# Kernel tuning notes

Hardware: AMD Instinct MI355X
Metric: run time of the kernel (lower is better)

The kernel has to match this reference:

```python
import jax, jax.numpy as jnp
import numpy as np
import math

D_MODEL, D_STATE, D_CONV = 1024, 16, 4
D_INNER = 2 * D_MODEL
DT_RANK = math.ceil(D_MODEL / 16)
B, L = 4, 2048


def setup_inputs() -> dict:
    key = jax.random.key(0)
    ks = jax.random.split(key, 10)
    s = 0.02
    x = jax.random.normal(ks[0], (B, L, D_MODEL), dtype=jnp.float32)
    ln_g = jnp.ones((D_MODEL,), jnp.float32)
    ln_b = jnp.zeros((D_MODEL,), jnp.float32)
    W_in = jax.random.normal(ks[1], (D_MODEL, 2 * D_INNER), jnp.float32) * s
    conv_w = jax.random.normal(ks[2], (D_INNER, 1, D_CONV), jnp.float32) * s
    conv_b = jnp.zeros((D_INNER,), jnp.float32)
    W_xp = jax.random.normal(ks[3], (D_INNER, DT_RANK + 2 * D_STATE), jnp.float32) * s
    W_dt = jax.random.normal(ks[4], (DT_RANK, D_INNER), jnp.float32) * (DT_RANK ** -0.5)
    # inverse-softplus of dt ~ 0.01 (between dt_min=0.001 and dt_max=0.1)
    dt_bias = jnp.full((D_INNER,), float(np.log(np.expm1(0.01))), jnp.float32)
    # S4D-real init: A = 1..d_state per channel
    A_log = jnp.log(jnp.broadcast_to(jnp.arange(1, D_STATE + 1, dtype=jnp.float32), (D_INNER, D_STATE)))
    D_skip = jnp.ones((D_INNER,), jnp.float32)
    W_out = jax.random.normal(ks[5], (D_INNER, D_MODEL), jnp.float32) * s
    return dict(x=x, ln_g=ln_g, ln_b=ln_b, W_in=W_in, conv_w=conv_w, conv_b=conv_b,
                W_xp=W_xp, W_dt=W_dt, dt_bias=dt_bias, A_log=A_log, D_skip=D_skip, W_out=W_out)


def _layernorm(x, g, b, eps=1e-5):
    m = jnp.mean(x, axis=-1, keepdims=True)
    v = jnp.mean(jnp.square(x - m), axis=-1, keepdims=True)
    return (x - m) * jax.lax.rsqrt(v + eps) * g + b


def _mamba(xn, W_in, conv_w, conv_b, W_xp, W_dt, dt_bias, A_log, D_skip, W_out):
    # xn: [B, L, d_model]
    xz = xn @ W_in                                   # [B, L, 2*d_inner]
    xi, z = jnp.split(xz, 2, axis=-1)                # each [B, L, d_inner]
    # depthwise causal conv over sequence
    xi_t = jnp.transpose(xi, (0, 2, 1))              # [B, d_inner, L]
    xc = jax.lax.conv_general_dilated(
        xi_t, conv_w, window_strides=(1,), padding=[(D_CONV - 1, 0)],
        feature_group_count=D_INNER, dimension_numbers=('NCH', 'OIH', 'NCH'))
    xc = jnp.transpose(xc, (0, 2, 1)) + conv_b       # [B, L, d_inner]
    xc = jax.nn.silu(xc)
    # input-dependent dt, B, C
    x_dbl = xc @ W_xp                                # [B, L, dt_rank + 2*d_state]
    dt_lo, Bm, Cm = jnp.split(x_dbl, [DT_RANK, DT_RANK + D_STATE], axis=-1)
    delta = jax.nn.softplus(dt_lo @ W_dt + dt_bias)  # [B, L, d_inner]
    A = -jnp.exp(A_log)                              # [d_inner, d_state]

    def step(h, inp):
        dt_t, B_t, C_t, u_t = inp                    # [B,D], [B,N], [B,N], [B,D]
        dA = jnp.exp(dt_t[..., None] * A)            # [B, D, N]
        h = h * dA + (dt_t * u_t)[..., None] * B_t[:, None, :]
        y = jnp.einsum('bdn,bn->bd', h, C_t)
        return h, y

    h0 = jnp.zeros((xn.shape[0], D_INNER, D_STATE), xn.dtype)
    inputs = (jnp.transpose(delta, (1, 0, 2)), jnp.transpose(Bm, (1, 0, 2)),
              jnp.transpose(Cm, (1, 0, 2)), jnp.transpose(xc, (1, 0, 2)))
    _, ys = jax.lax.scan(step, h0, inputs)           # ys: [L, B, d_inner]
    y = jnp.transpose(ys, (1, 0, 2)) + xc * D_skip   # [B, L, d_inner]
    y = y * jax.nn.silu(z)
    return y @ W_out                                 # [B, L, d_model]


def reference(x, ln_g, ln_b, W_in, conv_w, conv_b, W_xp, W_dt, dt_bias, A_log, D_skip, W_out):
    xn = _layernorm(x, ln_g, ln_b)
    return _mamba(xn, W_in, conv_w, conv_b, W_xp, W_dt, dt_bias, A_log, D_skip, W_out) + x
```

## Files before the change

kernel.cpp:

```cpp
#include <hip/hip_runtime.h>

#define DM 1024
#define DI 2048
#define DS 16
#define DTR 64
#define LL 2048
#define NROW 8192

typedef unsigned short u16;
typedef unsigned int u32;
typedef __bf16 bf16x8 __attribute__((ext_vector_type(8)));
typedef float f32x4 __attribute__((ext_vector_type(4)));
typedef float v2f __attribute__((ext_vector_type(2)));

__device__ __forceinline__ float bf2f(u16 u) {
  unsigned int v = ((unsigned int)u) << 16;
  return __builtin_bit_cast(float, v);
}
__device__ __forceinline__ u16 f2bf(float f) {
  unsigned int x = __builtin_bit_cast(unsigned int, f);
  x = x + 0x7fffu + ((x >> 16) & 1u);
  return (u16)(x >> 16);
}
__device__ __forceinline__ float lo_bf(u32 v) { return __builtin_bit_cast(float, v << 16); }
__device__ __forceinline__ float hi_bf(u32 v) { return __builtin_bit_cast(float, v & 0xFFFF0000u); }
__device__ __forceinline__ u32 pack_bf(float a, float b) {
  return (u32)f2bf(a) | ((u32)f2bf(b) << 16);
}
__device__ __forceinline__ bool io_f32(const u16* lng) { return lng[0] == 0; }

__device__ __forceinline__ void async16(const void* g, void* l) {
  __builtin_amdgcn_global_load_lds(
      (const __attribute__((address_space(1))) unsigned int*)g,
      (__attribute__((address_space(3))) unsigned int*)l, 16, 0, 0);
}

__device__ __forceinline__ void pow16v(float e1, v2f* E) {
  float e2 = e1 * e1;
  v2f sq = {e2, e2};
  E[0] = (v2f){e1, e2};
#pragma unroll
  for (int k = 1; k < 8; k++) E[k] = E[k - 1] * sq;
}

__device__ void transpose_dev(const void* __restrict__ in, u16* __restrict__ out,
                              int R, int C, int Cp, int bx, int by, bool f32,
                              int tid, u16 (*tile)[33]) {
  int c0 = bx * 32, r0 = by * 32;
  int tx = tid & 31, ty = tid >> 5;
#pragma unroll
  for (int i = 0; i < 4; i++) {
    int r = r0 + ty + i * 8, c = c0 + tx;
    u16 v = 0;
    if (r < R && c < C) {
      if (f32) v = f2bf(((const float*)in)[(size_t)r * C + c]);
      else     v = ((const u16*)in)[(size_t)r * C + c];
    }
    tile[ty + i * 8][tx] = v;
  }
  __syncthreads();
#pragma unroll
  for (int i = 0; i < 4; i++) {
    int oc = c0 + ty + i * 8, orr = r0 + tx;
    if (oc < Cp && orr < R) out[(size_t)oc * R + orr] = tile[tx][ty + i * 8];
  }
}

__global__ __launch_bounds__(256) void prep_k(
    const void* __restrict__ W_in, u16* __restrict__ W_inT,
    const void* __restrict__ W_dt, u16* __restrict__ W_dtT,
    const void* __restrict__ W_xp, u16* __restrict__ W_xpT,
    const void* __restrict__ W_out, u16* __restrict__ W_outT,
    const void* __restrict__ x, const u16* __restrict__ g,
    const u16* __restrict__ b, u16* __restrict__ xn) {
  __shared__ u16 tile[32][33];
  __shared__ float rs_[4], rq_[4];
  bool f32 = io_f32(g);
  int tid = threadIdx.x;
  int bid = blockIdx.x;
  if (bid < 4096) {
    transpose_dev(W_in, W_inT, 1024, 4096, 4096, bid & 127, bid >> 7, f32, tid, tile);
    return;
  } else if (bid < 4224) {
    bid -= 4096;
    transpose_dev(W_dt, W_dtT, 64, 2048, 2048, bid & 63, bid >> 6, f32, tid, tile);
    return;
  } else if (bid < 4480) {
    bid -= 4224;
    transpose_dev(W_xp, W_xpT, 2048, 96, 128, bid & 3, bid >> 2, f32, tid, tile);
    return;
  } else if (bid < 6528) {
    bid -= 4480;
    transpose_dev(W_out, W_outT, 2048, 1024, 1024, bid & 31, bid >> 5, f32, tid, tile);
    return;
  }
  int row = bid - 6528;
  float f[4];
  if (f32) {
    float4 v = ((const float4*)((const float*)x + (size_t)row * DM))[tid];
    f[0] = v.x; f[1] = v.y; f[2] = v.z; f[3] = v.w;
  } else {
    ushort4 v = ((const ushort4*)((const u16*)x + (size_t)row * DM))[tid];
    f[0] = bf2f(v.x); f[1] = bf2f(v.y); f[2] = bf2f(v.z); f[3] = bf2f(v.w);
  }
  float s = f[0] + f[1] + f[2] + f[3];
  float q = f[0] * f[0] + f[1] * f[1] + f[2] * f[2] + f[3] * f[3];
#pragma unroll
  for (int off = 32; off; off >>= 1) {
    s += __shfl_down(s, off, 64);
    q += __shfl_down(q, off, 64);
  }
  int wid = tid >> 6, lane = tid & 63;
  if (lane == 0) { rs_[wid] = s; rq_[wid] = q; }
  __syncthreads();
  float ts = rs_[0] + rs_[1] + rs_[2] + rs_[3];
  float tq = rq_[0] + rq_[1] + rq_[2] + rq_[3];
  float mean = ts * (1.f / DM);
  float var = tq * (1.f / DM) - mean * mean;
  float inv = rsqrtf(var + 1e-5f);
  int c = tid * 4;
  ushort4 o;
  u16* po = (u16*)&o;
#pragma unroll
  for (int k = 0; k < 4; k++) {
    float gk = f32 ? ((const float*)g)[c + k] : bf2f(g[c + k]);
    float bk = f32 ? ((const float*)b)[c + k] : bf2f(b[c + k]);
    po[k] = f2bf((f[k] - mean) * inv * gk + bk);
  }
  ((ushort4*)(xn + (size_t)row * DM))[tid] = o;
}

template <int EPI>
__device__ __forceinline__ void gemm_body(const u16* __restrict__ A,
                                          const u16* __restrict__ BT,
                                          void* __restrict__ C,
                                          const void* __restrict__ extra,
                                          int M, int N, int Klen, int ldk,
                                          const u16* __restrict__ lng, int mOff,
                                          u16* ldsA, u16* ldsB) {
  int tid = threadIdx.x;
  int wid = tid >> 6, lane = tid & 63;
  int l15 = lane & 15, quad = lane >> 4;
  int bm = blockIdx.x * 128;
  int bn;
  const u16* Ae = A;
  const u16* Be = BT;
  float* Cpart = nullptr;
  if (EPI == 5) {
    bn = 0;
    int ky = blockIdx.y;
    Ae += (size_t)ky * Klen;
    Be += (size_t)ky * Klen;
    Cpart = (float*)C + (size_t)ky * M * N;
  } else {
    bn = blockIdx.y * 128;
  }
  int wrow = (wid >> 1) * 64, wcol = (wid & 1) * 64;

  f32x4 zero = {0.f, 0.f, 0.f, 0.f};
  f32x4 acc[4][4];
#pragma unroll
  for (int i = 0; i < 4; i++)
#pragma unroll
    for (int j = 0; j < 4; j++) acc[i][j] = zero;

  int row0 = tid >> 2;
  int colb = (tid & 3) * 16;
  const char* Ap0 = (const char*)Ae + ((size_t)(bm + row0) * ldk) * 2 + colb;
  const char* Ap1 = (const char*)Ae + ((size_t)(bm + row0 + 64) * ldk) * 2 + colb;
  const char* Bp0 = (const char*)Be + ((size_t)(bn + row0) * ldk) * 2 + colb;
  const char* Bp1 = (const char*)Be + ((size_t)(bn + row0 + 64) * ldk) * 2 + colb;
  u16* la = ldsA + wid * 512;
  u16* lb = ldsB + wid * 512;

  for (int k0 = 0; k0 < Klen; k0 += 64) {
    size_t kb = (size_t)k0 * 2;
    async16(Ap0 + kb, la);
    async16(Ap1 + kb, la + 2048);
    async16(Ap0 + kb + 64, la + 4096);
    async16(Ap1 + kb + 64, la + 6144);
    async16(Bp0 + kb, lb);
    async16(Bp1 + kb, lb + 2048);
    async16(Bp0 + kb + 64, lb + 4096);
    async16(Bp1 + kb + 64, lb + 6144);
    __syncthreads();
#pragma unroll
    for (int s = 0; s < 2; s++) {
      bf16x8 af[4], bfr[4];
#pragma unroll
      for (int i = 0; i < 4; i++)
        af[i] = *(const bf16x8*)&ldsA[s * 4096 + (wrow + i * 16 + l15) * 32 + quad * 8];
#pragma unroll
      for (int j = 0; j < 4; j++)
        bfr[j] = *(const bf16x8*)&ldsB[s * 4096 + (wcol + j * 16 + l15) * 32 + quad * 8];
#pragma unroll
      for (int i = 0; i < 4; i++)
#pragma unroll
        for (int j = 0; j < 4; j++)
          acc[i][j] = __builtin_amdgcn_mfma_f32_16x16x32_bf16(af[i], bfr[j], acc[i][j], 0, 0, 0);
    }
    __syncthreads();
  }

  bool f32 = (EPI == 2 || EPI == 3) ? io_f32(lng) : false;
  if ((EPI == 2 || EPI == 3) && !f32) {
    u16* tile = ldsA;
#pragma unroll
    for (int i = 0; i < 4; i++) {
#pragma unroll
      for (int j = 0; j < 4; j++) {
        int gn = bn + wcol + j * 16 + l15;
#pragma unroll
        for (int r = 0; r < 4; r++) {
          int lr = wrow + i * 16 + quad * 4 + r;
          float v = acc[i][j][r];
          if (EPI == 2) {
            v += bf2f(((const u16*)extra)[gn]);
            v = (v > 20.f) ? v : log1pf(__expf(v));
          } else {
            v += bf2f(((const u16*)extra)[(size_t)(bm + lr + mOff) * N + gn]);
          }
          tile[lr * 128 + wcol + j * 16 + l15] = f2bf(v);
        }
      }
    }
    __syncthreads();
#pragma unroll
    for (int g = 0; g < 8; g++) {
      int gi = g * 256 + tid;
      int row = gi >> 4, cg = gi & 15;
      uint4 v4 = *(const uint4*)&tile[row * 128 + cg * 8];
      *(uint4*)((u16*)C + (size_t)(bm + row + mOff) * N + bn + cg * 8) = v4;
    }
    return;
  }
#pragma unroll
  for (int i = 0; i < 4; i++) {
#pragma unroll
    for (int j = 0; j < 4; j++) {
      int gn = bn + wcol + j * 16 + l15;
#pragma unroll
      for (int r = 0; r < 4; r++) {
        int gm = bm + wrow + i * 16 + quad * 4 + r;
        float v = acc[i][j][r];
        if (EPI == 2) {
          float bias = ((const float*)extra)[gn];
          v += bias;
          float sp = (v > 20.f) ? v : log1pf(__expf(v));
          ((u16*)C)[(size_t)gm * N + gn] = f2bf(sp);
        } else if (EPI == 3) {
          size_t idx = (size_t)(gm + mOff) * N + gn;
          v += ((const float*)extra)[idx];
          ((float*)C)[idx] = v;
        } else {
          Cpart[(size_t)gm * N + gn] = v;
        }
      }
    }
  }
}

#define GEMM_WRAP(name, EPI)                                                        \
  __global__ __launch_bounds__(256) void name(                                      \
      const u16* __restrict__ A, const u16* __restrict__ BT, void* __restrict__ C,  \
      const void* __restrict__ extra, int M, int N, int Klen, int ldk,              \
      const u16* __restrict__ lng, int mOff) {                                      \
    __shared__ __align__(16) u16 lds[16384];                                        \
    gemm_body<EPI>(A, BT, C, extra, M, N, Klen, ldk, lng, mOff, lds, lds + 8192);   \
  }

GEMM_WRAP(gemm_xp_k, 5)
GEMM_WRAP(gemm_dt_k, 2)
GEMM_WRAP(gemm_out_k, 3)

__global__ __launch_bounds__(512, 2) void gemm_in256_k(
    const u16* __restrict__ A, const u16* __restrict__ BT,
    u16* __restrict__ C, u16* __restrict__ Z, int ldk, int Klen) {
  __shared__ __align__(16) u16 lds[65536];
  const int tid = threadIdx.x;
  const int wid = tid >> 6, lane = tid & 63;
  const int l15 = lane & 15, quad = lane >> 4;
  const int bm = blockIdx.x * 256, bn = blockIdx.y * 256;
  const int wrow = (wid >> 2) * 128;
  const int wcol = (wid & 3) * 64;

  const int srow = tid >> 3;
  const int sg = ((tid & 7) ^ (srow & 7)) * 8;
  const u16* Ag[4];
  const u16* Bg[4];
#pragma unroll
  for (int s = 0; s < 4; s++) {
    Ag[s] = A + (size_t)(bm + s * 64 + srow) * ldk + sg;
    Bg[s] = BT + (size_t)(bn + s * 64 + srow) * ldk + sg;
  }
  const int sdst = wid * 512;

  int rA[2], rB[2];
#pragma unroll
  for (int ks = 0; ks < 2; ks++) {
    int gsw = ((ks * 4 + quad) ^ (l15 & 7)) * 8;
    rA[ks] = (wrow + l15) * 64 + gsw;
    rB[ks] = 16384 + (wcol + l15) * 64 + gsw;
  }

  f32x4 acc[8][4];
  f32x4 zero = {0.f, 0.f, 0.f, 0.f};
#pragma unroll
  for (int i = 0; i < 8; i++)
#pragma unroll
    for (int j = 0; j < 4; j++) acc[i][j] = zero;

  const int NT = Klen >> 6;
  async16(Ag[0], &lds[sdst]);
  async16(Ag[1], &lds[4096 + sdst]);
  async16(Ag[2], &lds[8192 + sdst]);
  async16(Ag[3], &lds[12288 + sdst]);
  async16(Bg[0], &lds[16384 + sdst]);
  async16(Bg[1], &lds[20480 + sdst]);
  async16(Bg[2], &lds[24576 + sdst]);
  async16(Bg[3], &lds[28672 + sdst]);
  if (NT > 1) {
    async16(Ag[0] + 64, &lds[32768 + sdst]);
    async16(Ag[1] + 64, &lds[36864 + sdst]);
    async16(Ag[2] + 64, &lds[40960 + sdst]);
    async16(Ag[3] + 64, &lds[45056 + sdst]);
    async16(Bg[0] + 64, &lds[49152 + sdst]);
    async16(Bg[1] + 64, &lds[53248 + sdst]);
    async16(Bg[2] + 64, &lds[57344 + sdst]);
    async16(Bg[3] + 64, &lds[61440 + sdst]);
  }
  asm volatile("s_waitcnt vmcnt(8)" ::: "memory");
  __builtin_amdgcn_s_barrier();
  __builtin_amdgcn_sched_barrier(0);

  bf16x8 aLo[4][2], aHi[4][2], b0[2][2], b1[2][2];
#pragma unroll
  for (int mf = 0; mf < 4; mf++) {
    aLo[mf][0] = *(const bf16x8*)&lds[rA[0] + mf * 1024];
    aLo[mf][1] = *(const bf16x8*)&lds[rA[1] + mf * 1024];
  }
#pragma unroll
  for (int nf = 0; nf < 2; nf++)
#pragma unroll
    for (int ks = 0; ks < 2; ks++) {
      b0[nf][ks] = *(const bf16x8*)&lds[rB[ks] + nf * 1024];
      b1[nf][ks] = *(const bf16x8*)&lds[rB[ks] + (2 + nf) * 1024];
    }

  for (int t = 0; t < NT; ++t) {
    const int bb = (t & 1) << 15;
    const int nb = bb ^ 32768;
    const int k2 = (t + 2) << 6;
    const bool st1 = (t + 1 < NT), st2 = (t + 2 < NT);

    __builtin_amdgcn_s_setprio(1);
#pragma unroll
    for (int ks = 0; ks < 2; ks++)
#pragma unroll
      for (int mf = 0; mf < 4; mf++)
#pragma unroll
        for (int nf = 0; nf < 2; nf++)
          acc[mf][nf] = __builtin_amdgcn_mfma_f32_16x16x32_bf16(aLo[mf][ks], b0[nf][ks], acc[mf][nf], 0, 0, 0);
    __builtin_amdgcn_s_setprio(0);
#pragma unroll
    for (int mf = 0; mf < 4; mf++) {
      aHi[mf][0] = *(const bf16x8*)&lds[bb + rA[0] + 4096 + mf * 1024];
      aHi[mf][1] = *(const bf16x8*)&lds[bb + rA[1] + 4096 + mf * 1024];
    }
    __builtin_amdgcn_s_setprio(1);
#pragma unroll
    for (int ks = 0; ks < 2; ks++)
#pragma unroll
      for (int mf = 0; mf < 4; mf++)
#pragma unroll
        for (int nf = 0; nf < 2; nf++)
          acc[mf][2 + nf] = __builtin_amdgcn_mfma_f32_16x16x32_bf16(aLo[mf][ks], b1[nf][ks], acc[mf][2 + nf], 0, 0, 0);
    __builtin_amdgcn_s_setprio(0);

    asm volatile("s_waitcnt lgkmcnt(0)" ::: "memory");
    __builtin_amdgcn_sched_barrier(0);
    asm volatile("s_waitcnt vmcnt(0)" ::: "memory");
    __builtin_amdgcn_s_barrier();
    __builtin_amdgcn_sched_barrier(0);

    if (st2) {
      async16(Ag[0] + k2, &lds[bb + sdst]);
      async16(Ag[1] + k2, &lds[bb + 4096 + sdst]);
      async16(Ag[2] + k2, &lds[bb + 8192 + sdst]);
      async16(Ag[3] + k2, &lds[bb + 12288 + sdst]);
      async16(Bg[0] + k2, &lds[bb + 16384 + sdst]);
      async16(Bg[1] + k2, &lds[bb + 20480 + sdst]);
      async16(Bg[2] + k2, &lds[bb + 24576 + sdst]);
      async16(Bg[3] + k2, &lds[bb + 28672 + sdst]);
    }
    if (st1) {
#pragma unroll
      for (int mf = 0; mf < 4; mf++) {
        aLo[mf][0] = *(const bf16x8*)&lds[nb + rA[0] + mf * 1024];
        aLo[mf][1] = *(const bf16x8*)&lds[nb + rA[1] + mf * 1024];
      }
    }
    __builtin_amdgcn_s_setprio(1);
#pragma unroll
    for (int ks = 0; ks < 2; ks++)
#pragma unroll
      for (int mf = 0; mf < 4; mf++)
#pragma unroll
        for (int nf = 0; nf < 2; nf++)
          acc[4 + mf][nf] = __builtin_amdgcn_mfma_f32_16x16x32_bf16(aHi[mf][ks], b0[nf][ks], acc[4 + mf][nf], 0, 0, 0);
    __builtin_amdgcn_s_setprio(0);
    if (st1) {
#pragma unroll
      for (int nf = 0; nf < 2; nf++)
#pragma unroll
        for (int ks = 0; ks < 2; ks++)
          b0[nf][ks] = *(const bf16x8*)&lds[nb + rB[ks] + nf * 1024];
    }
    __builtin_amdgcn_s_setprio(1);
#pragma unroll
    for (int ks = 0; ks < 2; ks++)
#pragma unroll
      for (int mf = 0; mf < 4; mf++)
#pragma unroll
        for (int nf = 0; nf < 2; nf++)
          acc[4 + mf][2 + nf] = __builtin_amdgcn_mfma_f32_16x16x32_bf16(aHi[mf][ks], b1[nf][ks], acc[4 + mf][2 + nf], 0, 0, 0);
    __builtin_amdgcn_s_setprio(0);
    if (st1) {
#pragma unroll
      for (int nf = 0; nf < 2; nf++)
#pragma unroll
        for (int ks = 0; ks < 2; ks++)
          b1[nf][ks] = *(const bf16x8*)&lds[nb + rB[ks] + (2 + nf) * 1024];
    }
  }

#pragma unroll
  for (int i = 0; i < 8; i++) {
#pragma unroll
    for (int j = 0; j < 4; j++) {
      int gn = bn + wcol + j * 16 + l15;
#pragma unroll
      for (int r = 0; r < 4; r++) {
        int gm = bm + wrow + i * 16 + quad * 4 + r;
        float v = acc[i][j][r];
        if (gn < DI) {
          C[(size_t)gm * DI + gn] = f2bf(v);
        } else {
          float sv = v / (1.f + __expf(-v));
          Z[(size_t)gm * DI + (gn - DI)] = f2bf(sv);
        }
      }
    }
  }
}

__global__ __launch_bounds__(256) void conv4_k(const u16* __restrict__ xi,
                                               const void* __restrict__ cw,
                                               const void* __restrict__ cb,
                                               u16* __restrict__ xc,
                                               const u16* __restrict__ lng) {
  bool f32 = io_f32(lng);
  int idx = blockIdx.x * 256 + threadIdx.x;
  int c = idx & (DI - 1);
  int rq = idx >> 11;
  int l4 = (rq & (LL / 4 - 1)) * 4;
  int b = rq >> 9;
  float w[4], bias;
  if (f32) {
    float4 w4 = *(const float4*)((const float*)cw + (size_t)c * 4);
    w[0] = w4.x; w[1] = w4.y; w[2] = w4.z; w[3] = w4.w;
    bias = ((const float*)cb)[c];
  } else {
    ushort4 w4 = *(const ushort4*)((const u16*)cw + (size_t)c * 4);
    w[0] = bf2f(w4.x); w[1] = bf2f(w4.y); w[2] = bf2f(w4.z); w[3] = bf2f(w4.w);
    bias = bf2f(((const u16*)cb)[c]);
  }
  size_t base = ((size_t)(b * LL + l4)) * DI + c;
  float v[7];
#pragma unroll
  for (int j = 0; j < 7; j++) {
    int lj = l4 - 3 + j;
    v[j] = (lj >= 0) ? bf2f(xi[base + (size_t)(j - 3) * DI]) : 0.f;
  }
#pragma unroll
  for (int r = 0; r < 4; r++) {
    float acc = bias + v[r] * w[0] + v[r + 1] * w[1] + v[r + 2] * w[2] + v[r + 3] * w[3];
    float sv = acc / (1.f + __expf(-acc));
    xc[base + (size_t)r * DI] = f2bf(sv);
  }
}

__global__ __launch_bounds__(256) void reduce_dtlo_k(const float* __restrict__ Cpart,
                                                     float* __restrict__ xdbl,
                                                     u16* __restrict__ dtlo, int M) {
  int i = blockIdx.x * 256 + threadIdx.x;
  size_t MN = (size_t)M * 128;
  float v = Cpart[i] + Cpart[MN + i] + Cpart[2 * MN + i] + Cpart[3 * MN + i];
  xdbl[i] = v;
  int j = i & 127, m = i >> 7;
  if (j < 64) dtlo[(size_t)m * 64 + j] = f2bf(v);
}

__device__ __forceinline__ bool fastA(const void* A_log, bool f32, int d0) {
  bool fast = true;
#pragma unroll
  for (int c = 0; c < 2; c++)
    for (int n = 0; n < 16; n++) {
      float al = f32 ? ((const float*)A_log)[(d0 + c) * DS + n]
                     : bf2f(((const u16*)A_log)[(d0 + c) * DS + n]);
      float Av = __expf(al);
      fast = fast && (__builtin_fabsf(Av - (float)(n + 1)) <= 1e-3f * (n + 1));
    }
  return fast;
}

template <int S>
__global__ __launch_bounds__(256) void scan_p1(const u16* __restrict__ delta,
                                               const u16* __restrict__ xc,
                                               const float* __restrict__ xdbl,
                                               const void* __restrict__ A_log,
                                               const u16* __restrict__ lng,
                                               float* __restrict__ Pbuf,
                                               float* __restrict__ Lbuf,
                                               int NS) {
  bool f32 = io_f32(lng);
  int tid = threadIdx.x;
  int seg = blockIdx.x, dch = blockIdx.y, bL = blockIdx.z;
  int d0 = (dch * 256 + tid) * 2;
  size_t rb = (size_t)bL * LL;
  int l0 = seg * S;
  extern __shared__ float bc[];
#pragma unroll 2
  for (int i = tid; i < S * 4; i += 256) {
    int t = i >> 2, k = (i & 3) * 4;
    *(float4*)&bc[t * 16 + k] = *(const float4*)&xdbl[(rb + l0 + t) * 128 + 64 + k];
  }
  __syncthreads();
  size_t sb = ((((size_t)bL * NS + seg) * DI) + d0) * DS;
  const u32* dpu = (const u32*)(delta + (rb + l0) * DI + d0);
  const u32* upu = (const u32*)(xc + (rb + l0) * DI + d0);
  if (fastA(A_log, f32, d0)) {
    v2f h0[8], h1[8];
#pragma unroll
    for (int k = 0; k < 8; k++) { h0[k] = (v2f){0.f, 0.f}; h1[k] = (v2f){0.f, 0.f}; }
    float sum0 = 0.f, sum1 = 0.f;
    const int T = 8;
    for (int t0 = 0; t0 < S; t0 += T) {
      u32 dv[T], uv[T];
#pragma unroll
      for (int j = 0; j < T; j++) {
        dv[j] = dpu[j * (DI / 2)];
        uv[j] = upu[j * (DI / 2)];
      }
      dpu += T * (DI / 2);
      upu += T * (DI / 2);
#pragma unroll
      for (int j = 0; j < T; j++) {
        float dt0 = lo_bf(dv[j]), dt1 = hi_bf(dv[j]);
        float u0 = lo_bf(uv[j]), u1 = hi_bf(uv[j]);
        sum0 += dt0; sum1 += dt1;
        const v2f* B2 = (const v2f*)&bc[(t0 + j) * 16];
        v2f E[8];
        pow16v(__expf(-dt0), E);
        float com0 = dt0 * u0;
        v2f cv0 = {com0, com0};
#pragma unroll
        for (int k = 0; k < 8; k++) h0[k] = h0[k] * E[k] + B2[k] * cv0;
        pow16v(__expf(-dt1), E);
        float com1 = dt1 * u1;
        v2f cv1 = {com1, com1};
#pragma unroll
        for (int k = 0; k < 8; k++) h1[k] = h1[k] * E[k] + B2[k] * cv1;
      }
    }
    v2f P[8];
    pow16v(__expf(-sum0), P);
#pragma unroll
    for (int k = 0; k < 8; k++) { *(v2f*)&Pbuf[sb + 2 * k] = P[k]; *(v2f*)&Lbuf[sb + 2 * k] = h0[k]; }
    pow16v(__expf(-sum1), P);
#pragma unroll
    for (int k = 0; k < 8; k++) { *(v2f*)&Pbuf[sb + 16 + 2 * k] = P[k]; *(v2f*)&Lbuf[sb + 16 + 2 * k] = h1[k]; }
  } else {
    for (int c = 0; c < 2; c++) {
      int d = d0 + c;
      float A2[16], h[16], P[16];
#pragma unroll
      for (int n = 0; n < 16; n++) {
        float al = f32 ? ((const float*)A_log)[d * DS + n] : bf2f(((const u16*)A_log)[d * DS + n]);
        A2[n] = -__expf(al);
        h[n] = 0.f; P[n] = 1.f;
      }
      const u16* dp = delta + (rb + l0) * DI + d;
      const u16* up = xc + (rb + l0) * DI + d;
      for (int t = 0; t < S; t++) {
        float dt = bf2f(dp[(size_t)t * DI]);
        float u = bf2f(up[(size_t)t * DI]);
        float com = dt * u;
        const float* Bf = &bc[t * 16];
#pragma unroll
        for (int n = 0; n < 16; n++) {
          float dA = __expf(dt * A2[n]);
          h[n] = fmaf(h[n], dA, com * Bf[n]);
          P[n] *= dA;
        }
      }
#pragma unroll
      for (int n = 0; n < 16; n++) { Pbuf[sb + 16 * c + n] = P[n]; Lbuf[sb + 16 * c + n] = h[n]; }
    }
  }
}

__global__ __launch_bounds__(256) void scan_p2(float* __restrict__ Pbuf,
                                               float* __restrict__ Lbuf, int NS) {
  int idx = blockIdx.x * 256 + threadIdx.x;
  int bL = idx >> 15;
  int dn = idx & 32767;
  float H = 0.f;
  for (int s = 0; s < NS; s++) {
    size_t o = ((size_t)(bL * NS + s) << 15) + dn;
    float P = Pbuf[o], Lv = Lbuf[o];
    Lbuf[o] = H;
    H = fmaf(P, H, Lv);
  }
}

template <int S>
__global__ __launch_bounds__(256) void scan_p3(u16* __restrict__ dy,
                                               const u16* __restrict__ xc,
                                               const float* __restrict__ xdbl,
                                               const u16* __restrict__ z,
                                               const void* __restrict__ A_log,
                                               const void* __restrict__ D_skip,
                                               const u16* __restrict__ lng,
                                               const float* __restrict__ Lbuf,
                                               int NS) {
  bool f32 = io_f32(lng);
  int tid = threadIdx.x;
  int seg = blockIdx.x, dch = blockIdx.y, bL = blockIdx.z;
  int d0 = (dch * 256 + tid) * 2;
  size_t rb = (size_t)bL * LL;
  int l0 = seg * S;
  extern __shared__ float bc[];
#pragma unroll 2
  for (int i = tid; i < S * 8; i += 256) {
    int t = i >> 3, k = (i & 7) * 4;
    *(float4*)&bc[t * 32 + k] = *(const float4*)&xdbl[(rb + l0 + t) * 128 + 64 + k];
  }
  __syncthreads();
  size_t sb = ((((size_t)bL * NS + seg) * DI) + d0) * DS;
  float Dv0 = f32 ? ((const float*)D_skip)[d0] : bf2f(((const u16*)D_skip)[d0]);
  float Dv1 = f32 ? ((const float*)D_skip)[d0 + 1] : bf2f(((const u16*)D_skip)[d0 + 1]);
  u32* dpu = (u32*)(dy + (rb + l0) * DI + d0);
  const u32* upu = (const u32*)(xc + (rb + l0) * DI + d0);
  const u32* zpu = (const u32*)(z + (rb + l0) * DI + d0);
  if (fastA(A_log, f32, d0)) {
    v2f h0[8], h1[8];
#pragma unroll
    for (int k = 0; k < 8; k++) {
      h0[k] = *(const v2f*)&Lbuf[sb + 2 * k];
      h1[k] = *(const v2f*)&Lbuf[sb + 16 + 2 * k];
    }
    const int T = 8;
    for (int t0 = 0; t0 < S; t0 += T) {
      u32 dv[T], uv[T], zv[T];
#pragma unroll
      for (int j = 0; j < T; j++) {
        dv[j] = dpu[j * (DI / 2)];
        uv[j] = upu[j * (DI / 2)];
        zv[j] = zpu[j * (DI / 2)];
      }
      upu += T * (DI / 2);
      zpu += T * (DI / 2);
#pragma unroll
      for (int j = 0; j < T; j++) {
        float dt0 = lo_bf(dv[j]), dt1 = hi_bf(dv[j]);
        float u0 = lo_bf(uv[j]), u1 = hi_bf(uv[j]);
        float zg0 = lo_bf(zv[j]), zg1 = hi_bf(zv[j]);
        const v2f* B2 = (const v2f*)&bc[(t0 + j) * 32];
        const v2f* C2 = (const v2f*)&bc[(t0 + j) * 32 + 16];
        v2f E[8];
        pow16v(__expf(-dt0), E);
        float com0 = dt0 * u0;
        v2f cv = {com0, com0};
        v2f a0 = {0.f, 0.f}, a1 = {0.f, 0.f};
#pragma unroll
        for (int k = 0; k < 8; k += 2) {
          h0[k] = h0[k] * E[k] + B2[k] * cv;
          h0[k + 1] = h0[k + 1] * E[k + 1] + B2[k + 1] * cv;
          a0 += h0[k] * C2[k];
          a1 += h0[k + 1] * C2[k + 1];
        }
        float cs0 = (a0.x + a0.y) + (a1.x + a1.y);
        pow16v(__expf(-dt1), E);
        float com1 = dt1 * u1;
        cv = (v2f){com1, com1};
        a0 = (v2f){0.f, 0.f}; a1 = (v2f){0.f, 0.f};
#pragma unroll
        for (int k = 0; k < 8; k += 2) {
          h1[k] = h1[k] * E[k] + B2[k] * cv;
          h1[k + 1] = h1[k + 1] * E[k + 1] + B2[k + 1] * cv;
          a0 += h1[k] * C2[k];
          a1 += h1[k + 1] * C2[k + 1];
        }
        float cs1 = (a0.x + a0.y) + (a1.x + a1.y);
        float y0 = (cs0 + u0 * Dv0) * zg0;
        float y1 = (cs1 + u1 * Dv1) * zg1;
        dpu[j * (DI / 2)] = pack_bf(y0, y1);
      }
      dpu += T * (DI / 2);
    }
  } else {
    for (int c = 0; c < 2; c++) {
      int d = d0 + c;
      float A2[16], h[16];
#pragma unroll
      for (int n = 0; n < 16; n++) {
        float al = f32 ? ((const float*)A_log)[d * DS + n] : bf2f(((const u16*)A_log)[d * DS + n]);
        A2[n] = -__expf(al);
        h[n] = Lbuf[sb + 16 * c + n];
      }
      float Dv = (c == 0) ? Dv0 : Dv1;
      u16* dp = dy + (rb + l0) * DI + d;
      const u16* up = xc + (rb + l0) * DI + d;
      const u16* zp = z + (rb + l0) * DI + d;
      for (int t = 0; t < S; t++) {
        float dt = bf2f(dp[(size_t)t * DI]);
        float u = bf2f(up[(size_t)t * DI]);
        float zg = bf2f(zp[(size_t)t * DI]);
        float com = dt * u;
        const float* Bf = &bc[t * 32];
        const float* Cf = &bc[t * 32 + 16];
        float cs = 0.f;
#pragma unroll
        for (int n = 0; n < 16; n++) {
          float dA = __expf(dt * A2[n]);
          h[n] = fmaf(h[n], dA, com * Bf[n]);
          cs = fmaf(h[n], Cf[n], cs);
        }
        dp[(size_t)t * DI] = f2bf((cs + u * Dv) * zg);
      }
    }
  }
}

static void launch_scan(int NS, int nb, u16* xi, u16* xc, float* xdbl, u16* z,
                        const u16* A_log, const u16* D_sk, const u16* ln_g,
                        float* Pbuf, float* Lbuf, hipStream_t stream) {
  int S = LL / NS;
  dim3 g1(NS, 4, nb);
  if (S == 32) {
    scan_p1<32><<<g1, 256, 32 * 64, stream>>>(xi, xc, xdbl, A_log, ln_g, Pbuf, Lbuf, NS);
  } else if (S == 64) {
    scan_p1<64><<<g1, 256, 64 * 64, stream>>>(xi, xc, xdbl, A_log, ln_g, Pbuf, Lbuf, NS);
  } else {
    scan_p1<128><<<g1, 256, 128 * 64, stream>>>(xi, xc, xdbl, A_log, ln_g, Pbuf, Lbuf, NS);
  }
  scan_p2<<<nb * 128, 256, 0, stream>>>(Pbuf, Lbuf, NS);
  if (S == 32) {
    scan_p3<32><<<g1, 256, 32 * 128, stream>>>(xi, xc, xdbl, z, A_log, D_sk, ln_g, Lbuf, NS);
  } else if (S == 64) {
    scan_p3<64><<<g1, 256, 64 * 128, stream>>>(xi, xc, xdbl, z, A_log, D_sk, ln_g, Lbuf, NS);
  } else {
    scan_p3<128><<<g1, 256, 128 * 128, stream>>>(xi, xc, xdbl, z, A_log, D_sk, ln_g, Lbuf, NS);
  }
}

extern "C" void kernel_launch(void* const* d_in, const int* in_sizes, int n_in,
                              void* d_out, int out_size, void* d_ws, size_t ws_size,
                              hipStream_t stream) {
  const u16* x = (const u16*)d_in[0];
  const u16* ln_g = (const u16*)d_in[1];
  const u16* ln_b = (const u16*)d_in[2];
  const u16* W_in = (const u16*)d_in[3];
  const u16* cw = (const u16*)d_in[4];
  const u16* cb = (const u16*)d_in[5];
  const u16* W_xp = (const u16*)d_in[6];
  const u16* W_dt = (const u16*)d_in[7];
  const u16* dt_b = (const u16*)d_in[8];
  const u16* A_log = (const u16*)d_in[9];
  const u16* D_sk = (const u16*)d_in[10];
  const u16* W_out = (const u16*)d_in[11];

  char* ws = (char*)d_ws;
  const size_t MB = 1024 * 1024;

  if (ws_size >= 124 * MB) {
    int NS = (ws_size >= 180 * MB) ? 64 : (ws_size >= 144 * MB) ? 32 : 16;
    u16* xc = (u16*)(ws + 0);
    u16* xn = xc;
    u16* W_inT = (u16*)(ws + 16 * MB);
    u16* xi = (u16*)(ws + 32 * MB);
    u16* z = (u16*)(ws + 64 * MB);
    float* xdbl = (float*)(ws + 96 * MB);
    u16* dtlo = (u16*)(ws + 100 * MB);
    u16* W_xpT = (u16*)(ws + 101 * MB);
    u16* W_dtT = (u16*)(ws + 102 * MB);
    u16* W_outT = (u16*)(ws + 103 * MB);
    size_t stateSz = (size_t)NS * 4 * DI * DS * 4;
    float* Cpart = (float*)(ws + 107 * MB);
    float* Pbuf = (float*)(ws + 107 * MB);
    float* Lbuf = (float*)(ws + 107 * MB + stateSz);

    prep_k<<<6528 + NROW, 256, 0, stream>>>(W_in, W_inT, W_dt, W_dtT, W_xp, W_xpT,
                                            W_out, W_outT, x, ln_g, ln_b, xn);
    gemm_in256_k<<<dim3(NROW / 256, (2 * DI) / 256), 512, 0, stream>>>(xn, W_inT, xi, z, DM, DM);
    conv4_k<<<(NROW / 4 * DI) / 256, 256, 0, stream>>>(xi, cw, cb, xc, ln_g);
    gemm_xp_k<<<dim3(64, 4), 256, 0, stream>>>(xc, W_xpT, Cpart, nullptr, NROW, 128, 512, DI, ln_g, 0);
    reduce_dtlo_k<<<(NROW * 128) / 256, 256, 0, stream>>>(Cpart, xdbl, dtlo, NROW);
    gemm_dt_k<<<dim3(64, 16), 256, 0, stream>>>(dtlo, W_dtT, xi, dt_b, NROW, DI, DTR, DTR, ln_g, 0);
    launch_scan(NS, 4, xi, xc, xdbl, z, A_log, D_sk, ln_g, Pbuf, Lbuf, stream);
    gemm_out_k<<<dim3(64, 8), 256, 0, stream>>>(xi, W_outT, d_out, x, NROW, DM, DI, DI, ln_g, 0);
  } else {
    int NS = 32;
    u16* W_inT = (u16*)(ws + 0);
    u16* W_xpT = (u16*)(ws + 8 * MB);
    u16* W_dtT = (u16*)(ws + 9 * MB);
    u16* W_outT = (u16*)(ws + 10 * MB);
    u16* xn = (u16*)(ws + 14 * MB);
    u16* xi = (u16*)(ws + 30 * MB);
    u16* z = (u16*)(ws + 38 * MB);
    u16* xc = (u16*)(ws + 46 * MB);
    float* xdbl = (float*)(ws + 54 * MB);
    u16* dtlo = (u16*)(ws + 55 * MB);
    float* Cpart = (float*)(ws + 56 * MB);
    float* Pbuf = (float*)(ws + 56 * MB);
    float* Lbuf = (float*)(ws + 61 * MB);

    prep_k<<<6528 + NROW, 256, 0, stream>>>(W_in, W_inT, W_dt, W_dtT, W_xp, W_xpT,
                                            W_out, W_outT, x, ln_g, ln_b, xn);
    for (int b = 0; b < 4; b++) {
      const u16* xnb = xn + (size_t)b * LL * DM;
      gemm_in256_k<<<dim3(LL / 256, (2 * DI) / 256), 512, 0, stream>>>(xnb, W_inT, xi, z, DM, DM);
      conv4_k<<<(LL / 4 * DI) / 256, 256, 0, stream>>>(xi, cw, cb, xc, ln_g);
      gemm_xp_k<<<dim3(16, 4), 256, 0, stream>>>(xc, W_xpT, Cpart, nullptr, LL, 128, 512, DI, ln_g, 0);
      reduce_dtlo_k<<<(LL * 128) / 256, 256, 0, stream>>>(Cpart, xdbl, dtlo, LL);
      gemm_dt_k<<<dim3(16, 16), 256, 0, stream>>>(dtlo, W_dtT, xi, dt_b, LL, DI, DTR, DTR, ln_g, 0);
      launch_scan(NS, 1, xi, xc, xdbl, z, A_log, D_sk, ln_g, Pbuf, Lbuf, stream);
      gemm_out_k<<<dim3(16, 8), 256, 0, stream>>>(xi, W_outT, d_out, x, LL, DM, DI, DI, ln_g, b * LL);
    }
  }
}
```

Measured before the change: 498.2 us.

## Stage GEMM epilogue through LDS for coalesced stores; pass segment dt sums to scan

```diff
diff --git a/kernel.cpp b/kernel.cpp
--- a/kernel.cpp
+++ b/kernel.cpp
@@ -434,22 +434,34 @@
     }
   }
 
-#pragma unroll
-  for (int i = 0; i < 8; i++) {
-#pragma unroll
-    for (int j = 0; j < 4; j++) {
-      int gn = bn + wcol + j * 16 + l15;
-#pragma unroll
-      for (int r = 0; r < 4; r++) {
-        int gm = bm + wrow + i * 16 + quad * 4 + r;
-        float v = acc[i][j][r];
-        if (gn < DI) {
-          C[(size_t)gm * DI + gn] = f2bf(v);
-        } else {
-          float sv = v / (1.f + __expf(-v));
-          Z[(size_t)gm * DI + (gn - DI)] = f2bf(sv);
+  __syncthreads();
+  {
+    const bool isZ = (bn >= DI);
+#pragma unroll
+    for (int i = 0; i < 8; i++) {
+#pragma unroll
+      for (int j = 0; j < 4; j++) {
+        int lc = wcol + j * 16 + l15;
+        int gr = lc >> 3, go = lc & 7;
+#pragma unroll
+        for (int r = 0; r < 4; r++) {
+          int lr = wrow + i * 16 + quad * 4 + r;
+          float v = acc[i][j][r];
+          if (isZ) v = v / (1.f + __expf(-v));
+          int grs = gr ^ ((lr & 7) ^ ((lr >> 3) & 7));
+          lds[lr * 256 + grs * 8 + go] = f2bf(v);
         }
       }
+    }
+    __syncthreads();
+    u16* outp = isZ ? (Z + (size_t)bm * DI + (bn - DI)) : (C + (size_t)bm * DI + bn);
+#pragma unroll
+    for (int g = 0; g < 16; g++) {
+      int gi = g * 512 + tid;
+      int row = gi >> 5, cg = gi & 31;
+      int cgs = cg ^ ((row & 7) ^ ((row >> 3) & 7));
+      uint4 v4 = *(const uint4*)&lds[row * 256 + cgs * 8];
+      *(uint4*)(outp + (size_t)row * DI + cg * 8) = v4;
     }
   }
 }
@@ -522,6 +534,7 @@
                                                const u16* __restrict__ lng,
                                                float* __restrict__ Pbuf,
                                                float* __restrict__ Lbuf,
+                                               float* __restrict__ sumbuf,
                                                int NS) {
   bool f32 = io_f32(lng);
   int tid = threadIdx.x;
@@ -573,13 +586,19 @@
         for (int k = 0; k < 8; k++) h1[k] = h1[k] * E[k] + B2[k] * cv1;
       }
     }
-    v2f P[8];
-    pow16v(__expf(-sum0), P);
-#pragma unroll
-    for (int k = 0; k < 8; k++) { *(v2f*)&Pbuf[sb + 2 * k] = P[k]; *(v2f*)&Lbuf[sb + 2 * k] = h0[k]; }
-    pow16v(__expf(-sum1), P);
-#pragma unroll
-    for (int k = 0; k < 8; k++) { *(v2f*)&Pbuf[sb + 16 + 2 * k] = P[k]; *(v2f*)&Lbuf[sb + 16 + 2 * k] = h1[k]; }
+#pragma unroll
+    for (int k = 0; k < 8; k++) { *(v2f*)&Lbuf[sb + 2 * k] = h0[k]; *(v2f*)&Lbuf[sb + 16 + 2 * k] = h1[k]; }
+    if (sumbuf) {
+      *(v2f*)&sumbuf[((size_t)(bL * NS + seg)) * DI + d0] = (v2f){sum0, sum1};
+    } else {
+      v2f P[8];
+      pow16v(__expf(-sum0), P);
+#pragma unroll
+      for (int k = 0; k < 8; k++) *(v2f*)&Pbuf[sb + 2 * k] = P[k];
+      pow16v(__expf(-sum1), P);
+#pragma unroll
+      for (int k = 0; k < 8; k++) *(v2f*)&Pbuf[sb + 16 + 2 * k] = P[k];
+    }
   } else {
     for (int c = 0; c < 2; c++) {
       int d = d0 + c;
@@ -611,14 +630,26 @@
 }
 
 __global__ __launch_bounds__(256) void scan_p2(float* __restrict__ Pbuf,
-                                               float* __restrict__ Lbuf, int NS) {
+                                               float* __restrict__ Lbuf,
+                                               const float* __restrict__ sumbuf,
+                                               const void* __restrict__ A_log,
+                                               const u16* __restrict__ lng, int NS) {
   int idx = blockIdx.x * 256 + threadIdx.x;
   int bL = idx >> 15;
   int dn = idx & 32767;
+  int d = dn >> 4, n = dn & 15;
+  bool useSum = false;
+  if (sumbuf) {
+    bool f32 = io_f32(lng);
+    useSum = fastA(A_log, f32, d & ~1);
+  }
+  float np1 = (float)(n + 1);
   float H = 0.f;
   for (int s = 0; s < NS; s++) {
     size_t o = ((size_t)(bL * NS + s) << 15) + dn;
-    float P = Pbuf[o], Lv = Lbuf[o];
+    float Lv = Lbuf[o];
+    float P = useSum ? __expf(-sumbuf[((size_t)(bL * NS + s)) * DI + d] * np1)
+                     : Pbuf[o];
     Lbuf[o] = H;
     H = fmaf(P, H, Lv);
   }
@@ -745,17 +776,18 @@
 
 static void launch_scan(int NS, int nb, u16* xi, u16* xc, float* xdbl, u16* z,
                         const u16* A_log, const u16* D_sk, const u16* ln_g,
-                        float* Pbuf, float* Lbuf, hipStream_t stream) {
+                        float* Pbuf, float* Lbuf, float* sumbuf,
+                        hipStream_t stream) {
   int S = LL / NS;
   dim3 g1(NS, 4, nb);
   if (S == 32) {
-    scan_p1<32><<<g1, 256, 32 * 64, stream>>>(xi, xc, xdbl, A_log, ln_g, Pbuf, Lbuf, NS);
+    scan_p1<32><<<g1, 256, 32 * 64, stream>>>(xi, xc, xdbl, A_log, ln_g, Pbuf, Lbuf, sumbuf, NS);
   } else if (S == 64) {
-    scan_p1<64><<<g1, 256, 64 * 64, stream>>>(xi, xc, xdbl, A_log, ln_g, Pbuf, Lbuf, NS);
+    scan_p1<64><<<g1, 256, 64 * 64, stream>>>(xi, xc, xdbl, A_log, ln_g, Pbuf, Lbuf, sumbuf, NS);
   } else {
-    scan_p1<128><<<g1, 256, 128 * 64, stream>>>(xi, xc, xdbl, A_log, ln_g, Pbuf, Lbuf, NS);
-  }
-  scan_p2<<<nb * 128, 256, 0, stream>>>(Pbuf, Lbuf, NS);
+    scan_p1<128><<<g1, 256, 128 * 64, stream>>>(xi, xc, xdbl, A_log, ln_g, Pbuf, Lbuf, sumbuf, NS);
+  }
+  scan_p2<<<nb * 128, 256, 0, stream>>>(Pbuf, Lbuf, sumbuf, A_log, ln_g, NS);
   if (S == 32) {
     scan_p3<32><<<g1, 256, 32 * 128, stream>>>(xi, xc, xdbl, z, A_log, D_sk, ln_g, Lbuf, NS);
   } else if (S == 64) {
@@ -800,6 +832,7 @@
     float* Cpart = (float*)(ws + 107 * MB);
     float* Pbuf = (float*)(ws + 107 * MB);
     float* Lbuf = (float*)(ws + 107 * MB + stateSz);
+    float* sumbuf = (NS >= 32) ? (float*)(ws + 107 * MB + 2 * stateSz) : nullptr;
 
     prep_k<<<6528 + NROW, 256, 0, stream>>>(W_in, W_inT, W_dt, W_dtT, W_xp, W_xpT,
                                             W_out, W_outT, x, ln_g, ln_b, xn);
@@ -808,7 +841,7 @@
     gemm_xp_k<<<dim3(64, 4), 256, 0, stream>>>(xc, W_xpT, Cpart, nullptr, NROW, 128, 512, DI, ln_g, 0);
     reduce_dtlo_k<<<(NROW * 128) / 256, 256, 0, stream>>>(Cpart, xdbl, dtlo, NROW);
     gemm_dt_k<<<dim3(64, 16), 256, 0, stream>>>(dtlo, W_dtT, xi, dt_b, NROW, DI, DTR, DTR, ln_g, 0);
-    launch_scan(NS, 4, xi, xc, xdbl, z, A_log, D_sk, ln_g, Pbuf, Lbuf, stream);
+    launch_scan(NS, 4, xi, xc, xdbl, z, A_log, D_sk, ln_g, Pbuf, Lbuf, sumbuf, stream);
     gemm_out_k<<<dim3(64, 8), 256, 0, stream>>>(xi, W_outT, d_out, x, NROW, DM, DI, DI, ln_g, 0);
   } else {
     int NS = 32;
@@ -835,7 +868,7 @@
       gemm_xp_k<<<dim3(16, 4), 256, 0, stream>>>(xc, W_xpT, Cpart, nullptr, LL, 128, 512, DI, ln_g, 0);
       reduce_dtlo_k<<<(LL * 128) / 256, 256, 0, stream>>>(Cpart, xdbl, dtlo, LL);
       gemm_dt_k<<<dim3(16, 16), 256, 0, stream>>>(dtlo, W_dtT, xi, dt_b, LL, DI, DTR, DTR, ln_g, 0);
-      launch_scan(NS, 1, xi, xc, xdbl, z, A_log, D_sk, ln_g, Pbuf, Lbuf, stream);
+      launch_scan(NS, 1, xi, xc, xdbl, z, A_log, D_sk, ln_g, Pbuf, Lbuf, nullptr, stream);
       gemm_out_k<<<dim3(16, 8), 256, 0, stream>>>(xi, W_outT, d_out, x, LL, DM, DI, DI, ln_g, b * LL);
     }
   }
```

After: 492.6 us. About the same (-1.1%).
